# Optimization experiments

Hardware: AMD Instinct MI355X
Metric: run time of the kernel (lower is better)

The kernel has to match this reference:

```python
import jax, jax.numpy as jnp
import numpy as np

# Module hyperparameters (from init_kwargs / HGSELLayer defaults)
D_MODEL = 512
D_FF = 2048
N_EXPERTS = 64
K_ACTIVE = 2
N_HASHES = 4
LAYER_ID = 0
SALT = 0.0
BUCKET_SCALE = 8.0        # hash bucket width for projection-based hashing
CAPACITY_FACTOR = 1.25    # per-expert capacity slack (hash routing is near-uniform)


def setup_inputs() -> dict:
    key = jax.random.key(0)
    k0, k1, k2, k3 = jax.random.split(key, 4)
    B, S = 4, 2048
    hidden_states = jax.random.normal(k0, (B, S, D_MODEL), dtype=jnp.float32)
    # Fixed (non-learned) hash projection vectors of the MultiHashRouter
    W_hash = jax.random.normal(k1, (N_HASHES, D_MODEL), dtype=jnp.float32) / np.float32(np.sqrt(D_MODEL))
    # Expert bank parameters: per-expert MLP d_model -> d_ff -> d_model
    W1 = jax.random.normal(k2, (N_EXPERTS, D_MODEL, D_FF), dtype=jnp.float32) * np.float32(1.0 / np.sqrt(D_MODEL))
    b1 = jnp.zeros((N_EXPERTS, D_FF), dtype=jnp.float32)
    W2 = jax.random.normal(k3, (N_EXPERTS, D_FF, D_MODEL), dtype=jnp.float32) * np.float32(1.0 / np.sqrt(D_FF))
    b2 = jnp.zeros((N_EXPERTS, D_MODEL), dtype=jnp.float32)
    return {"hidden_states": hidden_states, "W_hash": W_hash, "W1": W1, "b1": b1, "W2": W2, "b2": b2}


def reference(hidden_states, W_hash, W1, b1, W2, b2):
    B, S, D = hidden_states.shape
    T = B * S
    x = hidden_states.reshape(T, D)

    # ---- MultiHashRouter: hash-based top-k expert selection (non-learned routing) ----
    scores = x @ W_hash.T                                   # [T, n_hashes]
    buckets = jnp.mod(
        jnp.floor(scores * BUCKET_SCALE + SALT).astype(jnp.int32) + LAYER_ID,
        N_EXPERTS,
    )                                                       # [T, n_hashes]
    selected = buckets[:, :K_ACTIVE]                        # [T, k]
    flat_e = selected.reshape(-1)                           # [T*k]

    # ---- Dispatch: capacity-bucketed gather into per-expert buffers ----
    C = int(np.ceil(T * K_ACTIVE / N_EXPERTS * CAPACITY_FACTOR))
    oh = jax.nn.one_hot(flat_e, N_EXPERTS, dtype=jnp.int32)          # [T*k, E]
    pos = jnp.sum((jnp.cumsum(oh, axis=0) - 1) * oh, axis=1)         # slot within expert
    valid = pos < C                                                   # [T*k]
    pos_c = jnp.clip(pos, 0, C - 1)
    x_rep = jnp.repeat(x, K_ACTIVE, axis=0)                           # [T*k, D]
    buf = jnp.zeros((N_EXPERTS, C, D), dtype=x.dtype).at[flat_e, pos_c].add(
        jnp.where(valid[:, None], x_rep, 0.0)
    )                                                                 # [E, C, D]

    # ---- ExpertBank: grouped per-expert MLP (gelu) ----
    h = jax.nn.gelu(jnp.einsum('ecd,edf->ecf', buf, W1) + b1[:, None, :], approximate=False)
    y = jnp.einsum('ecf,efd->ecd', h, W2) + b2[:, None, :]            # [E, C, D]

    # ---- Combine: gather back per token-expert pair, uniform mean over k ----
    out_pairs = jnp.where(valid[:, None], y[flat_e, pos_c], 0.0)      # [T*k, D]
    out = out_pairs.reshape(T, K_ACTIVE, D).mean(axis=1)              # [T, D]
    return out.reshape(B, S, D)
```

## Files before the change

### kernel.cpp

```cpp
#include <hip/hip_runtime.h>
#include <hip/hip_bf16.h>

#define T_TOK 8192
#define NSLOT 16384
#define DM 512
#define DF 2048
#define NEXP 64
#define CAP 320

typedef __bf16 bf16_t;
typedef __bf16 bf16x8 __attribute__((ext_vector_type(8)));
typedef float floatx4 __attribute__((ext_vector_type(4)));

__global__ __launch_bounds__(256) void k_scores(const float* __restrict__ x,
        const float* __restrict__ Wh, int* __restrict__ e_arr, int* __restrict__ inv)
{
    int tid = threadIdx.x;
    if (tid < 10) inv[blockIdx.x * 10 + tid] = -1;
    int wid = tid >> 6, lane = tid & 63;
    int t = blockIdx.x * 4 + wid;
    const float4* xp = (const float4*)(x + (size_t)t * DM);
    float4 x0 = xp[lane * 2], x1 = xp[lane * 2 + 1];
    const float4* w0p = (const float4*)(Wh);
    const float4* w1p = (const float4*)(Wh + DM);
    float4 a0 = w0p[lane * 2], a1 = w0p[lane * 2 + 1];
    float4 b0 = w1p[lane * 2], b1 = w1p[lane * 2 + 1];
    float s0 = x0.x*a0.x + x0.y*a0.y + x0.z*a0.z + x0.w*a0.w
             + x1.x*a1.x + x1.y*a1.y + x1.z*a1.z + x1.w*a1.w;
    float s1 = x0.x*b0.x + x0.y*b0.y + x0.z*b0.z + x0.w*b0.w
             + x1.x*b1.x + x1.y*b1.y + x1.z*b1.z + x1.w*b1.w;
    #pragma unroll
    for (int off = 32; off; off >>= 1) {
        s0 += __shfl_xor(s0, off);
        s1 += __shfl_xor(s1, off);
    }
    if (lane == 0) {
        int q0 = ((int)floorf(s0 * 8.0f)) & 63;
        int q1 = ((int)floorf(s1 * 8.0f)) & 63;
        e_arr[2 * t]     = q0;
        e_arr[2 * t + 1] = q1;
    }
}

__global__ __launch_bounds__(256) void k_hist(const int* __restrict__ e_arr,
        int* __restrict__ rank_arr, int* __restrict__ hist_g)
{
    __shared__ int se[256];
    __shared__ int hist[64];
    int tid = threadIdx.x;
    if (tid < 64) hist[tid] = 0;
    __syncthreads();
    int s = blockIdx.x * 256 + tid;
    int e = e_arr[s];
    se[tid] = e;
    atomicAdd(&hist[e], 1);
    __syncthreads();
    int cnt = 0;
    for (int j = 0; j < 255; ++j)
        if (j < tid && se[j] == e) cnt++;
    rank_arr[s] = cnt;
    if (tid < 64) hist_g[blockIdx.x * 64 + tid] = hist[tid];
}

__global__ __launch_bounds__(256) void k_pos(const int* __restrict__ e_arr,
        const int* __restrict__ rank_arr, const int* __restrict__ hist_g,
        int* __restrict__ pos_arr, int* __restrict__ inv)
{
    __shared__ int base[64][64];
    int tid = threadIdx.x;
    if (tid < 64) {
        int run = 0;
        for (int c = 0; c < 64; ++c) {
            base[c][tid] = run;
            run += hist_g[c * 64 + tid];
        }
    }
    __syncthreads();
    for (int i = 0; i < 64; ++i) {
        int s = i * 256 + tid;
        int e = e_arr[s];
        int p = base[s >> 8][e] + rank_arr[s];
        pos_arr[s] = p;
        if (p < CAP) inv[e * CAP + p] = s;
    }
}

__global__ __launch_bounds__(256) void k_buf(const float* __restrict__ x,
        const int* __restrict__ inv, bf16_t* __restrict__ buf)
{
    int tid = threadIdx.x;
    int r = blockIdx.x * 4 + (tid >> 6);
    int lane = tid & 63;
    int s = inv[r];
    union { uint4 u; bf16_t h[8]; } pk;
    if (s >= 0) {
        int t = s >> 1;
        const float* xr = x + (size_t)t * DM + lane * 8;
        float4 f0 = *(const float4*)xr;
        float4 f1 = *(const float4*)(xr + 4);
        pk.h[0] = (bf16_t)f0.x; pk.h[1] = (bf16_t)f0.y;
        pk.h[2] = (bf16_t)f0.z; pk.h[3] = (bf16_t)f0.w;
        pk.h[4] = (bf16_t)f1.x; pk.h[5] = (bf16_t)f1.y;
        pk.h[6] = (bf16_t)f1.z; pk.h[7] = (bf16_t)f1.w;
    } else {
        pk.u.x = 0; pk.u.y = 0; pk.u.z = 0; pk.u.w = 0;
    }
    *(uint4*)(buf + (size_t)r * DM + lane * 8) = pk.u;
}

template<int M_TOT, int N_DIM, int K_DIM, bool GELU, bool OUT_BF16>
__global__ __launch_bounds__(256) void gemm_expert(const bf16_t* __restrict__ A,
        const float* __restrict__ B, const float* __restrict__ bias,
        void* __restrict__ OutP)
{
    constexpr int MT = (M_TOT + 127) / 128;
    constexpr int NT = N_DIM / 128;
    int bx = blockIdx.x;
    int e  = bx / (MT * NT);
    int rem = bx % (MT * NT);
    int mt = rem / NT;
    int nt = rem % NT;

    const bf16_t* Ae = A + (size_t)e * M_TOT * K_DIM;
    const float*  Be = B + (size_t)e * K_DIM * N_DIM;
    const float*  be = bias + (size_t)e * N_DIM;

    __shared__ bf16_t As[128][72];
    __shared__ bf16_t Bs[128][72];

    int tid = threadIdx.x;
    int lane = tid & 63;
    int wid = tid >> 6;
    int wm = (wid >> 1) * 64;
    int wn = (wid & 1) * 64;
    int qm = lane & 15;
    int quad = lane >> 4;

    floatx4 acc[4][4];
    #pragma unroll
    for (int i = 0; i < 4; ++i)
        #pragma unroll
        for (int j = 0; j < 4; ++j) acc[i][j] = (floatx4)0.0f;

    int ac = tid & 7;
    int ar = tid >> 3;
    int bkg = tid & 7;
    int bn0 = (tid >> 3) * 4;

    for (int kk = 0; kk < K_DIM; kk += 64) {
        #pragma unroll
        for (int pr = 0; pr < 4; ++pr) {
            int row = pr * 32 + ar;
            int grow = mt * 128 + row;
            if (grow >= M_TOT) grow = M_TOT - 1;
            uint4 v = *(const uint4*)(Ae + (size_t)grow * K_DIM + kk + ac * 8);
            *(uint4*)(&As[row][ac * 8]) = v;
        }
        float4 bv[8];
        #pragma unroll
        for (int p = 0; p < 8; ++p) {
            int k = bkg * 8 + p;
            bv[p] = *(const float4*)(Be + (size_t)(kk + k) * N_DIM + nt * 128 + bn0);
        }
        #pragma unroll
        for (int i = 0; i < 4; ++i) {
            union { uint4 u; bf16_t h[8]; } pk;
            #pragma unroll
            for (int p = 0; p < 8; ++p)
                pk.h[p] = (bf16_t)(((const float*)&bv[p])[i]);
            *(uint4*)(&Bs[bn0 + i][bkg * 8]) = pk.u;
        }
        __syncthreads();
        #pragma unroll
        for (int ks = 0; ks < 2; ++ks) {
            bf16x8 af[4], bfr[4];
            #pragma unroll
            for (int i = 0; i < 4; ++i)
                af[i] = *(const bf16x8*)(&As[wm + i * 16 + qm][ks * 32 + quad * 8]);
            #pragma unroll
            for (int j = 0; j < 4; ++j)
                bfr[j] = *(const bf16x8*)(&Bs[wn + j * 16 + qm][ks * 32 + quad * 8]);
            #pragma unroll
            for (int i = 0; i < 4; ++i)
                #pragma unroll
                for (int j = 0; j < 4; ++j)
                    acc[i][j] = __builtin_amdgcn_mfma_f32_16x16x32_bf16(
                        af[i], bfr[j], acc[i][j], 0, 0, 0);
        }
        __syncthreads();
    }

    #pragma unroll
    for (int j = 0; j < 4; ++j) {
        int gn = nt * 128 + wn + j * 16 + qm;
        float bz = be[gn];
        #pragma unroll
        for (int i = 0; i < 4; ++i) {
            int rowBase = mt * 128 + wm + i * 16 + quad * 4;
            #pragma unroll
            for (int r = 0; r < 4; ++r) {
                int gm = rowBase + r;
                if (gm < M_TOT) {
                    float v = acc[i][j][r] + bz;
                    if (GELU) v = 0.5f * v * (1.0f + erff(v * 0.70710678118654752f));
                    size_t idx = (size_t)e * M_TOT * N_DIM + (size_t)gm * N_DIM + gn;
                    if (OUT_BF16) ((bf16_t*)OutP)[idx] = (bf16_t)v;
                    else          ((float*)OutP)[idx]  = v;
                }
            }
        }
    }
}

__global__ __launch_bounds__(256) void k_gather(const float* __restrict__ y,
        const int* __restrict__ e_arr, const int* __restrict__ pos_arr,
        float* __restrict__ out)
{
    int tid = threadIdx.x;
    int t = blockIdx.x * 4 + (tid >> 6);
    int lane = tid & 63;
    float a[8];
    #pragma unroll
    for (int i = 0; i < 8; ++i) a[i] = 0.0f;
    #pragma unroll
    for (int k = 0; k < 2; ++k) {
        int s = 2 * t + k;
        int e = e_arr[s], p = pos_arr[s];
        if (p < CAP) {
            const float* yr = y + ((size_t)e * CAP + p) * DM + lane * 8;
            float4 f0 = *(const float4*)yr;
            float4 f1 = *(const float4*)(yr + 4);
            a[0] += f0.x; a[1] += f0.y; a[2] += f0.z; a[3] += f0.w;
            a[4] += f1.x; a[5] += f1.y; a[6] += f1.z; a[7] += f1.w;
        }
    }
    float4 o0, o1;
    o0.x = a[0] * 0.5f; o0.y = a[1] * 0.5f; o0.z = a[2] * 0.5f; o0.w = a[3] * 0.5f;
    o1.x = a[4] * 0.5f; o1.y = a[5] * 0.5f; o1.z = a[6] * 0.5f; o1.w = a[7] * 0.5f;
    float* orow = out + (size_t)t * DM + lane * 8;
    *(float4*)orow = o0;
    *(float4*)(orow + 4) = o1;
}

extern "C" void kernel_launch(void* const* d_in, const int* in_sizes, int n_in,
                              void* d_out, int out_size, void* d_ws, size_t ws_size,
                              hipStream_t stream)
{
    const float* x  = (const float*)d_in[0];
    const float* Wh = (const float*)d_in[1];
    const float* W1 = (const float*)d_in[2];
    const float* b1 = (const float*)d_in[3];
    const float* W2 = (const float*)d_in[4];
    const float* b2 = (const float*)d_in[5];
    float* out = (float*)d_out;

    char* p = (char*)d_ws;
    int*    e_arr  = (int*)p;    p += (size_t)NSLOT * 4;
    int*    rank_a = (int*)p;    p += (size_t)NSLOT * 4;
    int*    hist_g = (int*)p;    p += (size_t)64 * 64 * 4;
    int*    pos_a  = (int*)p;    p += (size_t)NSLOT * 4;
    int*    inv    = (int*)p;    p += (size_t)NEXP * CAP * 4;
    bf16_t* buf    = (bf16_t*)p; p += (size_t)NEXP * CAP * DM * 2;
    bf16_t* hbuf   = (bf16_t*)p; p += (size_t)NEXP * CAP * DF * 2;
    float*  ybuf   = (float*)p;  p += (size_t)NEXP * CAP * DM * 4;

    k_scores<<<2048, 256, 0, stream>>>(x, Wh, e_arr, inv);
    k_hist<<<64, 256, 0, stream>>>(e_arr, rank_a, hist_g);
    k_pos<<<1, 256, 0, stream>>>(e_arr, rank_a, hist_g, pos_a, inv);
    k_buf<<<NEXP * CAP / 4, 256, 0, stream>>>(x, inv, buf);
    gemm_expert<CAP, DF, DM, true,  true ><<<NEXP * 3 * (DF / 128), 256, 0, stream>>>(buf, W1, b1, (void*)hbuf);
    gemm_expert<CAP, DM, DF, false, false><<<NEXP * 3 * (DM / 128), 256, 0, stream>>>(hbuf, W2, b2, (void*)ybuf);
    k_gather<<<2048, 256, 0, stream>>>(ybuf, e_arr, pos_a, out);
}
```

Measured before the change: 838.1 us.

## Pre-transpose weights to bf16 and load GEMM tiles directly into LDS

Adds a per-call kernel that converts each expert's fp32 weights into a transposed bf16 copy, run once before each grouped GEMM. The GEMM then streams both operands with global_load_lds into XOR-swizzled LDS tiles, replacing the per-tile fp32 load, convert and scatter of B. Expert activation buffers are padded to 384 rows so tile loads need no row clamping. The trade-off is extra global traffic, since weights are read as fp32 and written back as bf16 before the GEMM reads them again, in exchange for a much lighter GEMM inner loop.

```diff
diff --git a/kernel.cpp b/kernel.cpp
--- a/kernel.cpp
+++ b/kernel.cpp
@@ -7,10 +7,17 @@
 #define DF 2048
 #define NEXP 64
 #define CAP 320
+#define MP 384
 
 typedef __bf16 bf16_t;
 typedef __bf16 bf16x8 __attribute__((ext_vector_type(8)));
 typedef float floatx4 __attribute__((ext_vector_type(4)));
+
+__device__ __forceinline__ void load_lds16(const bf16_t* g, bf16_t* l) {
+    __builtin_amdgcn_global_load_lds(
+        (const __attribute__((address_space(1))) void*)g,
+        (__attribute__((address_space(3))) void*)l, 16, 0, 0);
+}
 
 __global__ __launch_bounds__(256) void k_scores(const float* __restrict__ x,
         const float* __restrict__ Wh, int* __restrict__ e_arr, int* __restrict__ inv)
@@ -91,7 +98,8 @@
     int tid = threadIdx.x;
     int r = blockIdx.x * 4 + (tid >> 6);
     int lane = tid & 63;
-    int s = inv[r];
+    int e = r / MP, row = r % MP;
+    int s = (row < CAP) ? inv[e * CAP + row] : -1;
     union { uint4 u; bf16_t h[8]; } pk;
     if (s >= 0) {
         int t = s >> 1;
@@ -108,9 +116,46 @@
     *(uint4*)(buf + (size_t)r * DM + lane * 8) = pk.u;
 }
 
-template<int M_TOT, int N_DIM, int K_DIM, bool GELU, bool OUT_BF16>
-__global__ __launch_bounds__(256) void gemm_expert(const bf16_t* __restrict__ A,
-        const float* __restrict__ B, const float* __restrict__ bias,
+template<int K_DIM, int N_DIM>
+__global__ __launch_bounds__(256) void k_tcvt(const float* __restrict__ W,
+                                              bf16_t* __restrict__ WT)
+{
+    constexpr int KT = K_DIM / 64, NTT = N_DIM / 64;
+    int b = blockIdx.x;
+    int e = b / (KT * NTT);
+    int rem = b % (KT * NTT);
+    int kt = rem / NTT, nb = rem % NTT;
+    const float* We = W + (size_t)e * K_DIM * N_DIM;
+    bf16_t* Oe = WT + (size_t)e * N_DIM * K_DIM;
+    __shared__ float tile[64][68];
+    int tid = threadIdx.x;
+    {
+        int kl = tid >> 2, ng = (tid & 3) * 16;
+        const float* src = We + (size_t)(kt * 64 + kl) * N_DIM + nb * 64 + ng;
+        float4 v0 = ((const float4*)src)[0];
+        float4 v1 = ((const float4*)src)[1];
+        float4 v2 = ((const float4*)src)[2];
+        float4 v3 = ((const float4*)src)[3];
+        *(float4*)&tile[kl][ng]      = v0;
+        *(float4*)&tile[kl][ng + 4]  = v1;
+        *(float4*)&tile[kl][ng + 8]  = v2;
+        *(float4*)&tile[kl][ng + 12] = v3;
+    }
+    __syncthreads();
+    {
+        int nl = tid >> 2, kg = (tid & 3) * 16;
+        union { uint4 u[2]; bf16_t h[16]; } pk;
+        #pragma unroll
+        for (int i = 0; i < 16; ++i) pk.h[i] = (bf16_t)tile[kg + i][nl];
+        bf16_t* dst = Oe + (size_t)(nb * 64 + nl) * K_DIM + kt * 64 + kg;
+        *(uint4*)dst       = pk.u[0];
+        *(uint4*)(dst + 8) = pk.u[1];
+    }
+}
+
+template<int M_TOT, int OSTR, int N_DIM, int K_DIM, bool GELU, bool OUT_BF16>
+__global__ __launch_bounds__(256) void gemm_tc(const bf16_t* __restrict__ A,
+        const bf16_t* __restrict__ B, const float* __restrict__ bias,
         void* __restrict__ OutP)
 {
     constexpr int MT = (M_TOT + 127) / 128;
@@ -121,20 +166,23 @@
     int mt = rem / NT;
     int nt = rem % NT;
 
-    const bf16_t* Ae = A + (size_t)e * M_TOT * K_DIM;
-    const float*  Be = B + (size_t)e * K_DIM * N_DIM;
+    const bf16_t* Ae = A + (size_t)e * MP * K_DIM + (size_t)mt * 128 * K_DIM;
+    const bf16_t* Be = B + (size_t)e * N_DIM * K_DIM + (size_t)nt * 128 * K_DIM;
     const float*  be = bias + (size_t)e * N_DIM;
 
-    __shared__ bf16_t As[128][72];
-    __shared__ bf16_t Bs[128][72];
+    __shared__ __align__(16) bf16_t As[128 * 64];
+    __shared__ __align__(16) bf16_t Bs[128 * 64];
 
     int tid = threadIdx.x;
     int lane = tid & 63;
     int wid = tid >> 6;
+    int qm = lane & 15;
+    int quad = lane >> 4;
     int wm = (wid >> 1) * 64;
     int wn = (wid & 1) * 64;
-    int qm = lane & 15;
-    int quad = lane >> 4;
+
+    int srow = lane >> 3;
+    int gl = (lane & 7) ^ srow;
 
     floatx4 acc[4][4];
     #pragma unroll
@@ -142,44 +190,30 @@
         #pragma unroll
         for (int j = 0; j < 4; ++j) acc[i][j] = (floatx4)0.0f;
 
-    int ac = tid & 7;
-    int ar = tid >> 3;
-    int bkg = tid & 7;
-    int bn0 = (tid >> 3) * 4;
-
     for (int kk = 0; kk < K_DIM; kk += 64) {
         #pragma unroll
-        for (int pr = 0; pr < 4; ++pr) {
-            int row = pr * 32 + ar;
-            int grow = mt * 128 + row;
-            if (grow >= M_TOT) grow = M_TOT - 1;
-            uint4 v = *(const uint4*)(Ae + (size_t)grow * K_DIM + kk + ac * 8);
-            *(uint4*)(&As[row][ac * 8]) = v;
-        }
-        float4 bv[8];
-        #pragma unroll
-        for (int p = 0; p < 8; ++p) {
-            int k = bkg * 8 + p;
-            bv[p] = *(const float4*)(Be + (size_t)(kk + k) * N_DIM + nt * 128 + bn0);
-        }
-        #pragma unroll
-        for (int i = 0; i < 4; ++i) {
-            union { uint4 u; bf16_t h[8]; } pk;
-            #pragma unroll
-            for (int p = 0; p < 8; ++p)
-                pk.h[p] = (bf16_t)(((const float*)&bv[p])[i]);
-            *(uint4*)(&Bs[bn0 + i][bkg * 8]) = pk.u;
+        for (int c = 0; c < 4; ++c) {
+            int q = wid * 4 + c;
+            int row = q * 8 + srow;
+            load_lds16(Ae + (size_t)row * K_DIM + kk + gl * 8, As + q * 512);
+            load_lds16(Be + (size_t)row * K_DIM + kk + gl * 8, Bs + q * 512);
         }
         __syncthreads();
         #pragma unroll
         for (int ks = 0; ks < 2; ++ks) {
             bf16x8 af[4], bfr[4];
             #pragma unroll
-            for (int i = 0; i < 4; ++i)
-                af[i] = *(const bf16x8*)(&As[wm + i * 16 + qm][ks * 32 + quad * 8]);
+            for (int i = 0; i < 4; ++i) {
+                int r = wm + i * 16 + qm;
+                int pg = r * 8 + ((ks * 4 + quad) ^ (r & 7));
+                af[i] = *(const bf16x8*)(As + pg * 8);
+            }
             #pragma unroll
-            for (int j = 0; j < 4; ++j)
-                bfr[j] = *(const bf16x8*)(&Bs[wn + j * 16 + qm][ks * 32 + quad * 8]);
+            for (int j = 0; j < 4; ++j) {
+                int r = wn + j * 16 + qm;
+                int pg = r * 8 + ((ks * 4 + quad) ^ (r & 7));
+                bfr[j] = *(const bf16x8*)(Bs + pg * 8);
+            }
             #pragma unroll
             for (int i = 0; i < 4; ++i)
                 #pragma unroll
@@ -203,7 +237,7 @@
                 if (gm < M_TOT) {
                     float v = acc[i][j][r] + bz;
                     if (GELU) v = 0.5f * v * (1.0f + erff(v * 0.70710678118654752f));
-                    size_t idx = (size_t)e * M_TOT * N_DIM + (size_t)gm * N_DIM + gn;
+                    size_t idx = ((size_t)e * OSTR + gm) * N_DIM + gn;
                     if (OUT_BF16) ((bf16_t*)OutP)[idx] = (bf16_t)v;
                     else          ((float*)OutP)[idx]  = v;
                 }
@@ -260,15 +294,23 @@
     int*    hist_g = (int*)p;    p += (size_t)64 * 64 * 4;
     int*    pos_a  = (int*)p;    p += (size_t)NSLOT * 4;
     int*    inv    = (int*)p;    p += (size_t)NEXP * CAP * 4;
-    bf16_t* buf    = (bf16_t*)p; p += (size_t)NEXP * CAP * DM * 2;
-    bf16_t* hbuf   = (bf16_t*)p; p += (size_t)NEXP * CAP * DF * 2;
+    bf16_t* buf    = (bf16_t*)p;
     float*  ybuf   = (float*)p;  p += (size_t)NEXP * CAP * DM * 4;
+    bf16_t* hbuf   = (bf16_t*)p; p += (size_t)NEXP * MP * DF * 2;
+    bf16_t* wT     = (bf16_t*)p; p += (size_t)NEXP * DM * DF * 2;
 
     k_scores<<<2048, 256, 0, stream>>>(x, Wh, e_arr, inv);
     k_hist<<<64, 256, 0, stream>>>(e_arr, rank_a, hist_g);
     k_pos<<<1, 256, 0, stream>>>(e_arr, rank_a, hist_g, pos_a, inv);
-    k_buf<<<NEXP * CAP / 4, 256, 0, stream>>>(x, inv, buf);
-    gemm_expert<CAP, DF, DM, true,  true ><<<NEXP * 3 * (DF / 128), 256, 0, stream>>>(buf, W1, b1, (void*)hbuf);
-    gemm_expert<CAP, DM, DF, false, false><<<NEXP * 3 * (DM / 128), 256, 0, stream>>>(hbuf, W2, b2, (void*)ybuf);
+    k_buf<<<NEXP * MP / 4, 256, 0, stream>>>(x, inv, buf);
+
+    k_tcvt<DM, DF><<<NEXP * (DM / 64) * (DF / 64), 256, 0, stream>>>(W1, wT);
+    gemm_tc<CAP, MP, DF, DM, true, true>
+        <<<NEXP * 3 * (DF / 128), 256, 0, stream>>>(buf, wT, b1, (void*)hbuf);
+
+    k_tcvt<DF, DM><<<NEXP * (DF / 64) * (DM / 64), 256, 0, stream>>>(W2, wT);
+    gemm_tc<CAP, CAP, DM, DF, false, false>
+        <<<NEXP * 3 * (DM / 128), 256, 0, stream>>>(hbuf, wT, b2, (void*)ybuf);
+
     k_gather<<<2048, 256, 0, stream>>>(ybuf, e_arr, pos_a, out);
 }
```

Measured after the change: 916.7 us. 9.4% more time.

## Register-prefetch GEMM tiles, swizzle LDS, pad expert rows, parallelize position kernel

Applied to the files above, without the earlier changes.

Reworks the expert GEMM to load the next K-tile's A and B into registers while the current tile is computed. It stores tiles into LDS with an XOR swizzle to avoid bank conflicts and swaps the MFMA operands so the epilogue writes vectorized float4/bf16x4 rows. Expert buffers are padded to 384 rows, so GEMM A loads no longer need clamping, and the A buffer aliases the y buffer to save workspace. The single-block position kernel is split into 64 blocks. The changes add register pressure and a more complex indexing scheme.

```diff
diff --git a/kernel.cpp b/kernel.cpp
--- a/kernel.cpp
+++ b/kernel.cpp
@@ -7,6 +7,7 @@
 #define DF 2048
 #define NEXP 64
 #define CAP 320
+#define MP 384
 
 typedef __bf16 bf16_t;
 typedef __bf16 bf16x8 __attribute__((ext_vector_type(8)));
@@ -66,23 +67,19 @@
         const int* __restrict__ rank_arr, const int* __restrict__ hist_g,
         int* __restrict__ pos_arr, int* __restrict__ inv)
 {
-    __shared__ int base[64][64];
-    int tid = threadIdx.x;
+    __shared__ int base[64];
+    int tid = threadIdx.x, c = blockIdx.x;
     if (tid < 64) {
         int run = 0;
-        for (int c = 0; c < 64; ++c) {
-            base[c][tid] = run;
-            run += hist_g[c * 64 + tid];
-        }
+        for (int cc = 0; cc < c; ++cc) run += hist_g[cc * 64 + tid];
+        base[tid] = run;
     }
     __syncthreads();
-    for (int i = 0; i < 64; ++i) {
-        int s = i * 256 + tid;
-        int e = e_arr[s];
-        int p = base[s >> 8][e] + rank_arr[s];
-        pos_arr[s] = p;
-        if (p < CAP) inv[e * CAP + p] = s;
-    }
+    int s = c * 256 + tid;
+    int e = e_arr[s];
+    int p = base[e] + rank_arr[s];
+    pos_arr[s] = p;
+    if (p < CAP) inv[e * CAP + p] = s;
 }
 
 __global__ __launch_bounds__(256) void k_buf(const float* __restrict__ x,
@@ -91,7 +88,8 @@
     int tid = threadIdx.x;
     int r = blockIdx.x * 4 + (tid >> 6);
     int lane = tid & 63;
-    int s = inv[r];
+    int e = r / MP, row = r % MP;
+    int s = (row < CAP) ? inv[e * CAP + row] : -1;
     union { uint4 u; bf16_t h[8]; } pk;
     if (s >= 0) {
         int t = s >> 1;
@@ -108,8 +106,8 @@
     *(uint4*)(buf + (size_t)r * DM + lane * 8) = pk.u;
 }
 
-template<int M_TOT, int N_DIM, int K_DIM, bool GELU, bool OUT_BF16>
-__global__ __launch_bounds__(256) void gemm_expert(const bf16_t* __restrict__ A,
+template<int M_TOT, int OSTR, int N_DIM, int K_DIM, bool GELU, bool OUT_BF16>
+__global__ __launch_bounds__(256) void gemm_fused(const bf16_t* __restrict__ A,
         const float* __restrict__ B, const float* __restrict__ bias,
         void* __restrict__ OutP)
 {
@@ -121,20 +119,37 @@
     int mt = rem / NT;
     int nt = rem % NT;
 
-    const bf16_t* Ae = A + (size_t)e * M_TOT * K_DIM;
-    const float*  Be = B + (size_t)e * K_DIM * N_DIM;
-    const float*  be = bias + (size_t)e * N_DIM;
-
-    __shared__ bf16_t As[128][72];
-    __shared__ bf16_t Bs[128][72];
+    const bf16_t* Ae = A + (size_t)e * MP * K_DIM + (size_t)mt * 128 * K_DIM;
+    const float*  Be = B + (size_t)e * K_DIM * N_DIM + nt * 128;
+    const float*  be = bias + (size_t)e * N_DIM + nt * 128;
+
+    __shared__ __align__(16) bf16_t As[128 * 64];
+    __shared__ __align__(16) bf16_t Bs[128 * 64];
 
     int tid = threadIdx.x;
     int lane = tid & 63;
     int wid = tid >> 6;
+    int qm = lane & 15;
+    int quad = lane >> 4;
     int wm = (wid >> 1) * 64;
     int wn = (wid & 1) * 64;
-    int qm = lane & 15;
-    int quad = lane >> 4;
+
+    int srow = lane >> 3;
+    int gl = (lane & 7) ^ srow;
+    const bf16_t* aPtr = Ae + (size_t)(wid * 32 + srow) * K_DIM + gl * 8;
+
+    int bkg = tid & 7;
+    int bn  = (tid >> 3) * 4;
+    const float* bPtr = Be + (size_t)(bkg * 8) * N_DIM + bn;
+
+    uint4  aR[4];
+    float4 bR[8];
+    #pragma unroll
+    for (int c = 0; c < 4; ++c)
+        aR[c] = *(const uint4*)(aPtr + (size_t)c * 8 * K_DIM);
+    #pragma unroll
+    for (int p = 0; p < 8; ++p)
+        bR[p] = *(const float4*)(bPtr + (size_t)p * N_DIM);
 
     floatx4 acc[4][4];
     #pragma unroll
@@ -142,70 +157,78 @@
         #pragma unroll
         for (int j = 0; j < 4; ++j) acc[i][j] = (floatx4)0.0f;
 
-    int ac = tid & 7;
-    int ar = tid >> 3;
-    int bkg = tid & 7;
-    int bn0 = (tid >> 3) * 4;
-
+    #pragma unroll 2
     for (int kk = 0; kk < K_DIM; kk += 64) {
+        __syncthreads();
         #pragma unroll
-        for (int pr = 0; pr < 4; ++pr) {
-            int row = pr * 32 + ar;
-            int grow = mt * 128 + row;
-            if (grow >= M_TOT) grow = M_TOT - 1;
-            uint4 v = *(const uint4*)(Ae + (size_t)grow * K_DIM + kk + ac * 8);
-            *(uint4*)(&As[row][ac * 8]) = v;
-        }
-        float4 bv[8];
-        #pragma unroll
-        for (int p = 0; p < 8; ++p) {
-            int k = bkg * 8 + p;
-            bv[p] = *(const float4*)(Be + (size_t)(kk + k) * N_DIM + nt * 128 + bn0);
-        }
+        for (int c = 0; c < 4; ++c)
+            *(uint4*)(As + ((wid * 4 + c) * 64 + lane) * 8) = aR[c];
         #pragma unroll
         for (int i = 0; i < 4; ++i) {
             union { uint4 u; bf16_t h[8]; } pk;
             #pragma unroll
             for (int p = 0; p < 8; ++p)
-                pk.h[p] = (bf16_t)(((const float*)&bv[p])[i]);
-            *(uint4*)(&Bs[bn0 + i][bkg * 8]) = pk.u;
+                pk.h[p] = (bf16_t)(((const float*)&bR[p])[i]);
+            int r = bn + i;
+            *(uint4*)(Bs + ((r * 8 + (bkg ^ (r & 7))) * 8)) = pk.u;
+        }
+        if (kk + 64 < K_DIM) {
+            #pragma unroll
+            for (int c = 0; c < 4; ++c)
+                aR[c] = *(const uint4*)(aPtr + (size_t)c * 8 * K_DIM + (kk + 64));
+            #pragma unroll
+            for (int p = 0; p < 8; ++p)
+                bR[p] = *(const float4*)(bPtr + (size_t)(kk + 64 + p) * N_DIM);
         }
         __syncthreads();
         #pragma unroll
         for (int ks = 0; ks < 2; ++ks) {
             bf16x8 af[4], bfr[4];
             #pragma unroll
-            for (int i = 0; i < 4; ++i)
-                af[i] = *(const bf16x8*)(&As[wm + i * 16 + qm][ks * 32 + quad * 8]);
-            #pragma unroll
-            for (int j = 0; j < 4; ++j)
-                bfr[j] = *(const bf16x8*)(&Bs[wn + j * 16 + qm][ks * 32 + quad * 8]);
+            for (int i = 0; i < 4; ++i) {
+                int r = wm + i * 16 + qm;
+                int pg = r * 8 + ((ks * 4 + quad) ^ (r & 7));
+                af[i] = *(const bf16x8*)(As + pg * 8);
+            }
+            #pragma unroll
+            for (int j = 0; j < 4; ++j) {
+                int r = wn + j * 16 + qm;
+                int pg = r * 8 + ((ks * 4 + quad) ^ (r & 7));
+                bfr[j] = *(const bf16x8*)(Bs + pg * 8);
+            }
             #pragma unroll
             for (int i = 0; i < 4; ++i)
                 #pragma unroll
                 for (int j = 0; j < 4; ++j)
                     acc[i][j] = __builtin_amdgcn_mfma_f32_16x16x32_bf16(
-                        af[i], bfr[j], acc[i][j], 0, 0, 0);
-        }
-        __syncthreads();
-    }
-
-    #pragma unroll
-    for (int j = 0; j < 4; ++j) {
-        int gn = nt * 128 + wn + j * 16 + qm;
-        float bz = be[gn];
-        #pragma unroll
-        for (int i = 0; i < 4; ++i) {
-            int rowBase = mt * 128 + wm + i * 16 + quad * 4;
-            #pragma unroll
-            for (int r = 0; r < 4; ++r) {
-                int gm = rowBase + r;
-                if (gm < M_TOT) {
-                    float v = acc[i][j][r] + bz;
-                    if (GELU) v = 0.5f * v * (1.0f + erff(v * 0.70710678118654752f));
-                    size_t idx = (size_t)e * M_TOT * N_DIM + (size_t)gm * N_DIM + gn;
-                    if (OUT_BF16) ((bf16_t*)OutP)[idx] = (bf16_t)v;
-                    else          ((float*)OutP)[idx]  = v;
+                        bfr[j], af[i], acc[i][j], 0, 0, 0);
+        }
+    }
+
+    #pragma unroll
+    for (int i = 0; i < 4; ++i) {
+        int gm = mt * 128 + wm + i * 16 + qm;
+        if (gm < M_TOT) {
+            #pragma unroll
+            for (int j = 0; j < 4; ++j) {
+                int ln0 = wn + j * 16 + quad * 4;
+                float4 bz = *(const float4*)(be + ln0);
+                float v[4];
+                #pragma unroll
+                for (int r = 0; r < 4; ++r) {
+                    float t = acc[i][j][r] + ((const float*)&bz)[r];
+                    if (GELU) t = 0.5f * t * (1.0f + erff(t * 0.70710678118654752f));
+                    v[r] = t;
+                }
+                size_t idx = ((size_t)e * OSTR + gm) * N_DIM + nt * 128 + ln0;
+                if (OUT_BF16) {
+                    union { uint2 u; bf16_t h[4]; } pk;
+                    pk.h[0] = (bf16_t)v[0]; pk.h[1] = (bf16_t)v[1];
+                    pk.h[2] = (bf16_t)v[2]; pk.h[3] = (bf16_t)v[3];
+                    *(uint2*)((bf16_t*)OutP + idx) = pk.u;
+                } else {
+                    float4 o; o.x = v[0]; o.y = v[1]; o.z = v[2]; o.w = v[3];
+                    *(float4*)((float*)OutP + idx) = o;
                 }
             }
         }
@@ -260,15 +283,20 @@
     int*    hist_g = (int*)p;    p += (size_t)64 * 64 * 4;
     int*    pos_a  = (int*)p;    p += (size_t)NSLOT * 4;
     int*    inv    = (int*)p;    p += (size_t)NEXP * CAP * 4;
-    bf16_t* buf    = (bf16_t*)p; p += (size_t)NEXP * CAP * DM * 2;
-    bf16_t* hbuf   = (bf16_t*)p; p += (size_t)NEXP * CAP * DF * 2;
+    bf16_t* buf    = (bf16_t*)p;
     float*  ybuf   = (float*)p;  p += (size_t)NEXP * CAP * DM * 4;
+    bf16_t* hbuf   = (bf16_t*)p; p += (size_t)NEXP * MP * DF * 2;
 
     k_scores<<<2048, 256, 0, stream>>>(x, Wh, e_arr, inv);
     k_hist<<<64, 256, 0, stream>>>(e_arr, rank_a, hist_g);
-    k_pos<<<1, 256, 0, stream>>>(e_arr, rank_a, hist_g, pos_a, inv);
-    k_buf<<<NEXP * CAP / 4, 256, 0, stream>>>(x, inv, buf);
-    gemm_expert<CAP, DF, DM, true,  true ><<<NEXP * 3 * (DF / 128), 256, 0, stream>>>(buf, W1, b1, (void*)hbuf);
-    gemm_expert<CAP, DM, DF, false, false><<<NEXP * 3 * (DM / 128), 256, 0, stream>>>(hbuf, W2, b2, (void*)ybuf);
+    k_pos<<<64, 256, 0, stream>>>(e_arr, rank_a, hist_g, pos_a, inv);
+    k_buf<<<NEXP * MP / 4, 256, 0, stream>>>(x, inv, buf);
+
+    gemm_fused<CAP, MP, DF, DM, true, true>
+        <<<NEXP * 3 * (DF / 128), 256, 0, stream>>>(buf, W1, b1, (void*)hbuf);
+
+    gemm_fused<CAP, CAP, DM, DF, false, false>
+        <<<NEXP * 3 * (DM / 128), 256, 0, stream>>>(hbuf, W2, b2, (void*)ybuf);
+
     k_gather<<<2048, 256, 0, stream>>>(ybuf, e_arr, pos_a, out);
 }
```

Result: slower. 902.7 us (+7.7%).
